# Kernel tuning notes

Measured on AMD Instinct MI355X. Metric: run time of the kernel, lower is better.

## Reference

```python
import jax, jax.numpy as jnp
import numpy as np

B, N, S, D1, D2 = 16, 4096, 1024, 128, 256
MLP = [256, 128]
BN_EPS = 1e-5


def setup_inputs() -> dict:
    key = jax.random.key(0)
    ks = jax.random.split(key, 12)
    inp = {
        "xyz1": jax.random.normal(ks[0], (B, 3, N), dtype=jnp.float32),
        "xyz2": jax.random.normal(ks[1], (B, 3, S), dtype=jnp.float32),
        "points1": jax.random.normal(ks[2], (B, D1, N), dtype=jnp.float32),
        "points2": jax.random.normal(ks[3], (B, D2, S), dtype=jnp.float32),
    }
    in_ch = D1 + D2  # 384
    chans = [in_ch] + MLP
    ki = 4
    for li in range(len(MLP)):
        cin, cout = chans[li], chans[li + 1]
        inp[f"w{li+1}"] = jax.random.normal(ks[ki], (cout, cin), dtype=jnp.float32) * (1.0 / np.sqrt(cin)); ki += 1
        inp[f"b{li+1}"] = jnp.zeros((cout,), dtype=jnp.float32)
        inp[f"g{li+1}"] = jnp.ones((cout,), dtype=jnp.float32)
        inp[f"beta{li+1}"] = jnp.zeros((cout,), dtype=jnp.float32)
    return inp


def _batchnorm1d(x, gamma, beta):
    # x: [B, C, N]; training-mode batch stats over (B, N)
    mean = jnp.mean(x, axis=(0, 2), keepdims=True)
    var = jnp.var(x, axis=(0, 2), keepdims=True)
    xhat = (x - mean) * jax.lax.rsqrt(var + BN_EPS)
    return xhat * gamma[None, :, None] + beta[None, :, None]


def reference(xyz1, xyz2, points1, points2, w1, b1, g1, beta1, w2, b2, g2, beta2):
    x1 = jnp.transpose(xyz1, (0, 2, 1))   # [B, N, 3]
    x2 = jnp.transpose(xyz2, (0, 2, 1))   # [B, S, 3]
    p2 = jnp.transpose(points2, (0, 2, 1))  # [B, S, D2]

    # squared pairwise distances [B, N, S]
    dists = jnp.sum((x1[:, :, None, :] - x2[:, None, :, :]) ** 2, axis=-1)
    # 3 smallest distances (original sorts then slices top-3)
    neg_d3, idx = jax.lax.top_k(-dists, 3)  # [B, N, 3]
    d3 = -neg_d3
    dist_recip = 1.0 / (d3 + 1e-8)
    weight = dist_recip / jnp.sum(dist_recip, axis=2, keepdims=True)  # [B, N, 3]

    # gather neighbor features: [B, N, 3, D2]
    feats = p2[jnp.arange(p2.shape[0])[:, None, None], idx]
    interp = jnp.sum(feats * weight[..., None], axis=2)  # [B, N, D2]

    p1 = jnp.transpose(points1, (0, 2, 1))  # [B, N, D1]
    new_points = jnp.concatenate([p1, interp], axis=-1)  # [B, N, D1+D2]
    x = jnp.transpose(new_points, (0, 2, 1))  # [B, C, N]

    for w, b, g, bt in ((w1, b1, g1, beta1), (w2, b2, g2, beta2)):
        x = jnp.einsum("oc,bcn->bon", w, x) + b[None, :, None]
        x = _batchnorm1d(x, g, bt)
        x = jax.nn.relu(x)
    return x
```

## Files before the change

### kernel.cpp

```cpp
#include <hip/hip_runtime.h>

typedef unsigned short u16;
typedef unsigned int   u32;
typedef __attribute__((ext_vector_type(8))) short bf16x8;
typedef __attribute__((ext_vector_type(8))) unsigned short u16x8;
typedef __attribute__((ext_vector_type(4))) float f32x4;

#define NB   16
#define NPTS 4096
#define SPTS 1024
#define BNT  65536

__device__ __forceinline__ float bf2f(u16 u){ return __uint_as_float(((u32)u)<<16); }
__device__ __forceinline__ u16 f2bf(float f){
  u32 u = __float_as_uint(f);
  return (u16)((u + 0x7FFFu + ((u>>16)&1u))>>16);
}

__global__ __launch_bounds__(256) void convw_k(const float* __restrict__ w1, const float* __restrict__ w2,
                                               u16* __restrict__ w1b, u16* __restrict__ w2b){
  int i = blockIdx.x*256 + threadIdx.x;
  if (i < 98304) w1b[i] = f2bf(w1[i]);
  else { int j = i - 98304; w2b[j] = f2bf(w2[j]); }
}

__global__ __launch_bounds__(256) void transpose_k(const float* __restrict__ in, u16* __restrict__ out,
                                                   int C, int S, int ostride){
  __shared__ float tl[64][65];
  int t = threadIdx.x;
  int b = blockIdx.y;
  int s0 = blockIdx.x * 64;
  for (int ct = 0; ct < C; ct += 64){
    __syncthreads();
    for (int i = t; i < 4096; i += 256){
      int sl = i & 63, cl = i >> 6;
      tl[sl][cl] = in[((size_t)b*C + ct + cl)*S + s0 + sl];
    }
    __syncthreads();
    for (int i = t; i < 4096; i += 256){
      int cl = i & 63, sl = i >> 6;
      out[((size_t)b*S + s0 + sl)*ostride + ct + cl] = f2bf(tl[sl][cl]);
    }
  }
}

__global__ __launch_bounds__(512) void knn_k(const float* __restrict__ xyz1, const float* __restrict__ xyz2,
                                             const u16* __restrict__ p2t, u16* __restrict__ X){
  __shared__ float4 sxyz[SPTS];
  __shared__ float  pd[8][3][64];
  __shared__ int    pi[8][3][64];
  __shared__ float  swts[3][64];
  __shared__ int    sidx[3][64];
  int t  = threadIdx.x;
  int b  = blockIdx.x >> 6;
  int n0 = (blockIdx.x & 63) << 6;
  const float* x2b = xyz2 + (size_t)b*3*SPTS;
  for (int s = t; s < SPTS; s += 512)
    sxyz[s] = make_float4(x2b[s], x2b[SPTS+s], x2b[2*SPTS+s], 0.f);
  int q = t & 63, g = t >> 6;
  const float* x1b = xyz1 + (size_t)b*3*NPTS;
  int n = n0 + q;
  float qx = x1b[n], qy = x1b[NPTS+n], qz = x1b[2*NPTS+n];
  __syncthreads();

  float d0=3.4e38f, d1=3.4e38f, d2=3.4e38f;
  int   i0=0, i1=0, i2=0;
  int sBeg = g << 7, sEnd = sBeg + 128;
  for (int s = sBeg; s < sEnd; ++s){
    float4 p = sxyz[s];
    float dist;
    {
      #pragma clang fp contract(off)
      float dx = qx - p.x, dy = qy - p.y, dz = qz - p.z;
      dist = ((dx*dx) + (dy*dy)) + (dz*dz);
    }
    if (dist < d2){
      bool c1 = dist < d1, c0 = dist < d0;
      d2 = c1 ? d1 : dist;                 i2 = c1 ? i1 : s;
      float nd1 = c1 ? (c0 ? d0 : dist) : d1;
      int   ni1 = c1 ? (c0 ? i0 : s)    : i1;
      d0 = c0 ? dist : d0;                 i0 = c0 ? s : i0;
      d1 = nd1;                            i1 = ni1;
    }
  }
  pd[g][0][q]=d0; pd[g][1][q]=d1; pd[g][2][q]=d2;
  pi[g][0][q]=i0; pi[g][1][q]=i1; pi[g][2][q]=i2;
  __syncthreads();

  if (t < 64){
    float m0=3.4e38f, m1=3.4e38f, m2=3.4e38f;
    int   j0=0, j1=0, j2=0;
    #pragma unroll
    for (int gg = 0; gg < 8; ++gg){
      #pragma unroll
      for (int p = 0; p < 3; ++p){
        float dist = pd[gg][p][t]; int s = pi[gg][p][t];
        if (dist < m2){
          bool c1 = dist < m1, c0 = dist < m0;
          m2 = c1 ? m1 : dist;                 j2 = c1 ? j1 : s;
          float nd1 = c1 ? (c0 ? m0 : dist) : m1;
          int   ni1 = c1 ? (c0 ? j0 : s)    : j1;
          m0 = c0 ? dist : m0;                 j0 = c0 ? s : j0;
          m1 = nd1;                            j1 = ni1;
        }
      }
    }
    float r0 = 1.f/(m0 + 1e-8f), r1 = 1.f/(m1 + 1e-8f), r2 = 1.f/(m2 + 1e-8f);
    float rs = (r0 + r1) + r2;
    swts[0][t] = r0/rs; swts[1][t] = r1/rs; swts[2][t] = r2/rs;
    sidx[0][t] = j0;    sidx[1][t] = j1;    sidx[2][t] = j2;
  }
  __syncthreads();

  int w = t >> 6, lane = t & 63;
  for (int qq = w*8; qq < w*8 + 8; ++qq){
    float wa = swts[0][qq], wb = swts[1][qq], wc = swts[2][qq];
    int   j0 = sidx[0][qq], j1 = sidx[1][qq], j2 = sidx[2][qq];
    const ushort4 u0 = *(const ushort4*)(p2t + (((size_t)b*SPTS + j0)<<8) + (lane<<2));
    const ushort4 u1 = *(const ushort4*)(p2t + (((size_t)b*SPTS + j1)<<8) + (lane<<2));
    const ushort4 u2 = *(const ushort4*)(p2t + (((size_t)b*SPTS + j2)<<8) + (lane<<2));
    ushort4 ov;
    ov.x = f2bf(wa*bf2f(u0.x) + wb*bf2f(u1.x) + wc*bf2f(u2.x));
    ov.y = f2bf(wa*bf2f(u0.y) + wb*bf2f(u1.y) + wc*bf2f(u2.y));
    ov.z = f2bf(wa*bf2f(u0.z) + wb*bf2f(u1.z) + wc*bf2f(u2.z));
    ov.w = f2bf(wa*bf2f(u0.w) + wb*bf2f(u1.w) + wc*bf2f(u2.w));
    *(ushort4*)(X + ((size_t)b*NPTS + n0 + qq)*384 + 128 + (lane<<2)) = ov;
  }
}


__global__ __launch_bounds__(256) void gemm1_k(const u16* __restrict__ A, const u16* __restrict__ Bw,
                                               u16* __restrict__ Cc,
                                               float* __restrict__ psum, float* __restrict__ psq){
  const int K = 384, Nn = 256;
  __shared__ u16 lA[64*64];
  __shared__ u16 lB[128*64];
  __shared__ float sums[128], sqs[128];
  int t = threadIdx.x, lane = t & 63, wid = t >> 6;
  int rowBase = blockIdx.x << 6, colBase = blockIdx.y << 7;
  int wm = wid >> 1, wn = wid & 1;

  const char* pA[2]; char* dA[2];
  #pragma unroll
  for (int j = 0; j < 2; ++j){
    int L = j*4096 + wid*1024 + lane*16;
    int row = L >> 7, kb = L & 127;
    int kbs = kb ^ ((row & 7) << 4);
    pA[j] = (const char*)A + ((size_t)(rowBase + row)*K)*2 + kbs;
    dA[j] = (char*)lA + j*4096 + wid*1024;
  }
  const char* pB[4]; char* dB[4];
  #pragma unroll
  for (int j = 0; j < 4; ++j){
    int L = j*4096 + wid*1024 + lane*16;
    int row = L >> 7, kb = L & 127;
    int kbs = kb ^ ((row & 7) << 4);
    pB[j] = (const char*)Bw + ((size_t)(colBase + row)*K)*2 + kbs;
    dB[j] = (char*)lB + j*4096 + wid*1024;
  }

  f32x4 z = {0.f,0.f,0.f,0.f};
  f32x4 acc[2][4];
  #pragma unroll
  for (int m = 0; m < 2; ++m)
    #pragma unroll
    for (int n = 0; n < 4; ++n) acc[m][n] = z;

  for (int kk = 0; kk < K; kk += 64){
    size_t ko = (size_t)kk * 2;
    #pragma unroll
    for (int j = 0; j < 2; ++j)
      __builtin_amdgcn_global_load_lds((const __attribute__((address_space(1))) void*)(pA[j] + ko),
                                       (__attribute__((address_space(3))) void*)dA[j], 16, 0, 0);
    #pragma unroll
    for (int j = 0; j < 4; ++j)
      __builtin_amdgcn_global_load_lds((const __attribute__((address_space(1))) void*)(pB[j] + ko),
                                       (__attribute__((address_space(3))) void*)dB[j], 16, 0, 0);
    __syncthreads();
    bf16x8 af[2][2], bfv[4][2];
    #pragma unroll
    for (int m = 0; m < 2; ++m){
      int row = wm*32 + m*16 + (lane & 15);
      int sw = (row & 7) << 4;
      #pragma unroll
      for (int ks = 0; ks < 2; ++ks){
        int kb = (ks*64 + ((lane >> 4) << 4)) ^ sw;
        af[m][ks] = *(const bf16x8*)((const char*)lA + row*128 + kb);
      }
    }
    #pragma unroll
    for (int n = 0; n < 4; ++n){
      int row = wn*64 + n*16 + (lane & 15);
      int sw = (row & 7) << 4;
      #pragma unroll
      for (int ks = 0; ks < 2; ++ks){
        int kb = (ks*64 + ((lane >> 4) << 4)) ^ sw;
        bfv[n][ks] = *(const bf16x8*)((const char*)lB + row*128 + kb);
      }
    }
    #pragma unroll
    for (int ks = 0; ks < 2; ++ks)
      #pragma unroll
      for (int m = 0; m < 2; ++m)
        #pragma unroll
        for (int n = 0; n < 4; ++n)
          acc[m][n] = __builtin_amdgcn_mfma_f32_16x16x32_bf16(af[m][ks], bfv[n][ks], acc[m][n], 0, 0, 0);
    __syncthreads();
  }

  if (t < 128){ sums[t] = 0.f; sqs[t] = 0.f; }
  __syncthreads();
  int colb = colBase + wn*64 + (lane & 15);
  int rowb = rowBase + wm*32 + ((lane >> 4) << 2);
  #pragma unroll
  for (int n = 0; n < 4; ++n){
    float s = 0.f, qq2 = 0.f;
    #pragma unroll
    for (int m = 0; m < 2; ++m){
      #pragma unroll
      for (int r = 0; r < 4; ++r){
        float v = acc[m][n][r];
        Cc[(size_t)(rowb + m*16 + r)*Nn + colb + n*16] = f2bf(v);
        s += v; qq2 += v*v;
      }
    }
    atomicAdd(&sums[wn*64 + n*16 + (lane & 15)], s);
    atomicAdd(&sqs [wn*64 + n*16 + (lane & 15)], qq2);
  }
  __syncthreads();
  if (t < 128){
    int c = colBase + t;
    psum[(size_t)c*1024 + blockIdx.x] = sums[t];
    psq [(size_t)c*1024 + blockIdx.x] = sqs[t];
  }
}

__global__ __launch_bounds__(256) void gemm2_k(const u16* __restrict__ A, const u16* __restrict__ Bw,
                                               u16* __restrict__ Cc,
                                               const float* __restrict__ sc, const float* __restrict__ sh,
                                               float* __restrict__ psum, float* __restrict__ psq){
  const int K = 256, Nn = 128;
  __shared__ u16 lA[64*64];
  __shared__ u16 lB[128*64];
  __shared__ float sums[128], sqs[128];
  int t = threadIdx.x, lane = t & 63, wid = t >> 6;
  int rowBase = blockIdx.x << 6;
  int wm = wid >> 1, wn = wid & 1;

  const char* pB[4]; char* dB[4];
  #pragma unroll
  for (int j = 0; j < 4; ++j){
    int L = j*4096 + wid*1024 + lane*16;
    int row = L >> 7, kb = L & 127;
    int kbs = kb ^ ((row & 7) << 4);
    pB[j] = (const char*)Bw + ((size_t)row*K)*2 + kbs;
    dB[j] = (char*)lB + j*4096 + wid*1024;
  }
  int arow = t & 63, achunk = t >> 6;
  const u16* pArow = A + (size_t)(rowBase + arow)*K + achunk*16;
  int asw = (arow & 7) << 4;
  char* wA0 = (char*)lA + arow*128 + (((achunk*32)      ) ^ asw);
  char* wA1 = (char*)lA + arow*128 + (((achunk*32) + 16 ) ^ asw);

  f32x4 z = {0.f,0.f,0.f,0.f};
  f32x4 acc[2][4];
  #pragma unroll
  for (int m = 0; m < 2; ++m)
    #pragma unroll
    for (int n = 0; n < 4; ++n) acc[m][n] = z;

  for (int kk = 0; kk < K; kk += 64){
    size_t ko = (size_t)kk * 2;
    #pragma unroll
    for (int j = 0; j < 4; ++j)
      __builtin_amdgcn_global_load_lds((const __attribute__((address_space(1))) void*)(pB[j] + ko),
                                       (__attribute__((address_space(3))) void*)dB[j], 16, 0, 0);
    u16x8 y0 = *(const u16x8*)(pArow + kk);
    u16x8 y1 = *(const u16x8*)(pArow + kk + 8);
    int k0 = kk + achunk*16;
    bf16x8 o0, o1;
    #pragma unroll
    for (int j = 0; j < 8; ++j){
      float v = bf2f((u16)y0[j]) * sc[k0 + j] + sh[k0 + j];
      o0[j] = (short)f2bf(fmaxf(v, 0.f));
    }
    #pragma unroll
    for (int j = 0; j < 8; ++j){
      float v = bf2f((u16)y1[j]) * sc[k0 + 8 + j] + sh[k0 + 8 + j];
      o1[j] = (short)f2bf(fmaxf(v, 0.f));
    }
    *(bf16x8*)wA0 = o0;
    *(bf16x8*)wA1 = o1;
    __syncthreads();
    bf16x8 af[2][2], bfv[4][2];
    #pragma unroll
    for (int m = 0; m < 2; ++m){
      int row = wm*32 + m*16 + (lane & 15);
      int sw = (row & 7) << 4;
      #pragma unroll
      for (int ks = 0; ks < 2; ++ks){
        int kb = (ks*64 + ((lane >> 4) << 4)) ^ sw;
        af[m][ks] = *(const bf16x8*)((const char*)lA + row*128 + kb);
      }
    }
    #pragma unroll
    for (int n = 0; n < 4; ++n){
      int row = wn*64 + n*16 + (lane & 15);
      int sw = (row & 7) << 4;
      #pragma unroll
      for (int ks = 0; ks < 2; ++ks){
        int kb = (ks*64 + ((lane >> 4) << 4)) ^ sw;
        bfv[n][ks] = *(const bf16x8*)((const char*)lB + row*128 + kb);
      }
    }
    #pragma unroll
    for (int ks = 0; ks < 2; ++ks)
      #pragma unroll
      for (int m = 0; m < 2; ++m)
        #pragma unroll
        for (int n = 0; n < 4; ++n)
          acc[m][n] = __builtin_amdgcn_mfma_f32_16x16x32_bf16(af[m][ks], bfv[n][ks], acc[m][n], 0, 0, 0);
    __syncthreads();
  }

  if (t < 128){ sums[t] = 0.f; sqs[t] = 0.f; }
  __syncthreads();
  int colb = wn*64 + (lane & 15);
  int rowb = rowBase + wm*32 + ((lane >> 4) << 2);
  #pragma unroll
  for (int n = 0; n < 4; ++n){
    float s = 0.f, qq2 = 0.f;
    #pragma unroll
    for (int m = 0; m < 2; ++m){
      #pragma unroll
      for (int r = 0; r < 4; ++r){
        float v = acc[m][n][r];
        Cc[(size_t)(rowb + m*16 + r)*Nn + colb + n*16] = f2bf(v);
        s += v; qq2 += v*v;
      }
    }
    atomicAdd(&sums[colb + n*16], s);
    atomicAdd(&sqs [colb + n*16], qq2);
  }
  __syncthreads();
  if (t < 128){
    psum[(size_t)t*1024 + blockIdx.x] = sums[t];
    psq [(size_t)t*1024 + blockIdx.x] = sqs[t];
  }
}

__global__ __launch_bounds__(256) void finalize2_k(const float* __restrict__ psum, const float* __restrict__ psq,
                                                   const float* __restrict__ g, const float* __restrict__ bet,
                                                   float* __restrict__ sc, float* __restrict__ sh){
  __shared__ float rs[256], rq[256];
  int c = blockIdx.x, t = threadIdx.x;
  float s = 0.f, q = 0.f;
  for (int rt = t; rt < 1024; rt += 256){
    s += psum[(size_t)c*1024 + rt];
    q += psq [(size_t)c*1024 + rt];
  }
  rs[t] = s; rq[t] = q;
  __syncthreads();
  for (int off = 128; off; off >>= 1){
    if (t < off){ rs[t] += rs[t+off]; rq[t] += rq[t+off]; }
    __syncthreads();
  }
  if (t == 0){
    const float inv = 1.f/65536.f;
    float mean = rs[0]*inv;
    float var  = rq[0]*inv - mean*mean;
    float rstd = rsqrtf(var + 1e-5f);
    float scl  = g[c]*rstd;
    sc[c] = scl;
    sh[c] = bet[c] - mean*scl;
  }
}

__global__ __launch_bounds__(256) void finalout_k(const u16* __restrict__ y2, const float* __restrict__ sc,
                                                  const float* __restrict__ sh, float* __restrict__ out){
  __shared__ float tl[128][65];
  int t  = threadIdx.x;
  int b  = blockIdx.x >> 6;
  int n0 = (blockIdx.x & 63) << 6;
  for (int i = t; i < 8192; i += 256){
    int r = i >> 7, c = i & 127;
    float v = bf2f(y2[((size_t)b*NPTS + n0 + r)*128 + c]);
    v = fmaxf(v*sc[c] + sh[c], 0.f);
    tl[c][r] = v;
  }
  __syncthreads();
  for (int i = t; i < 8192; i += 256){
    int o = i >> 6, j = i & 63;
    out[(size_t)b*128*NPTS + (size_t)o*NPTS + n0 + j] = tl[o][j];
  }
}

extern "C" void kernel_launch(void* const* d_in, const int* in_sizes, int n_in,
                              void* d_out, int out_size, void* d_ws, size_t ws_size,
                              hipStream_t stream) {
  const float* xyz1    = (const float*)d_in[0];
  const float* xyz2    = (const float*)d_in[1];
  const float* points1 = (const float*)d_in[2];
  const float* points2 = (const float*)d_in[3];
  const float* w1      = (const float*)d_in[4];
  const float* g1      = (const float*)d_in[6];
  const float* beta1   = (const float*)d_in[7];
  const float* w2      = (const float*)d_in[8];
  const float* g2      = (const float*)d_in[10];
  const float* beta2   = (const float*)d_in[11];

  char* ws = (char*)d_ws;
  u16*  X    = (u16*)ws;
  u16*  Y2   = (u16*)ws;
  u16*  Y1   = (u16*)(ws + 50331648);
  u16*  p2t  = (u16*)(ws + 83886080);
  u16*  w1b  = (u16*)(ws + 92274688);
  u16*  w2b  = (u16*)(ws + 92471296);
  float* psum1 = (float*)(ws + 83886080);
  float* psq1  = (float*)(ws + 84934656);
  float* psum2 = (float*)(ws + 85983232);
  float* psq2  = (float*)(ws + 86507520);
  float* sc1   = (float*)(ws + 87031808);
  float* sh1   = (float*)(ws + 87032832);
  float* sc2   = (float*)(ws + 87033856);
  float* sh2   = (float*)(ws + 87034368);

  convw_k<<<512, 256, 0, stream>>>(w1, w2, w1b, w2b);
  transpose_k<<<dim3(64, 16), 256, 0, stream>>>(points1, X,   128, NPTS, 384);
  transpose_k<<<dim3(16, 16), 256, 0, stream>>>(points2, p2t, 256, SPTS, 256);
  knn_k<<<1024, 512, 0, stream>>>(xyz1, xyz2, p2t, X);
  gemm1_k<<<dim3(1024, 2), 256, 0, stream>>>(X, w1b, Y1, psum1, psq1);
  finalize2_k<<<256, 256, 0, stream>>>(psum1, psq1, g1, beta1, sc1, sh1);
  gemm2_k<<<1024, 256, 0, stream>>>(Y1, w2b, Y2, sc1, sh1, psum2, psq2);
  finalize2_k<<<128, 256, 0, stream>>>(psum2, psq2, g2, beta2, sc2, sh2);
  finalout_k<<<1024, 256, 0, stream>>>(Y2, sc2, sh2, (float*)d_out);
}
```

Measured before the change: 154.9 us.

## Double-buffer GEMM K-loops, widen gemm1 tile, pack kNN distance+index into doubles

Both GEMM kernels now double-buffer their LDS tiles, so the next K-slice is prefetched with global_load_lds while MFMAs run on the current one. gemm1 covers all 256 output columns per block, which halves the grid and removes the repeated A-tile loads. The kNN top-3 packs the distance and index into one double and keeps a branchless fmin/fmax sorting network. Costs are more LDS and registers per block, which may lower occupancy, and the packed index overwrites low mantissa bits, so near-equal distances can tie-break differently.

```diff
diff --git a/kernel.cpp b/kernel.cpp
--- a/kernel.cpp
+++ b/kernel.cpp
@@ -2,6 +2,7 @@
 
 typedef unsigned short u16;
 typedef unsigned int   u32;
+typedef unsigned long long u64;
 typedef __attribute__((ext_vector_type(8))) short bf16x8;
 typedef __attribute__((ext_vector_type(8))) unsigned short u16x8;
 typedef __attribute__((ext_vector_type(4))) float f32x4;
@@ -10,6 +11,10 @@
 #define NPTS 4096
 #define SPTS 1024
 #define BNT  65536
+
+#define G2L(src, dst) __builtin_amdgcn_global_load_lds( \
+    (const __attribute__((address_space(1))) void*)(src), \
+    (__attribute__((address_space(3))) void*)(dst), 16, 0, 0)
 
 __device__ __forceinline__ float bf2f(u16 u){ return __uint_as_float(((u32)u)<<16); }
 __device__ __forceinline__ u16 f2bf(float f){
@@ -47,8 +52,7 @@
 __global__ __launch_bounds__(512) void knn_k(const float* __restrict__ xyz1, const float* __restrict__ xyz2,
                                              const u16* __restrict__ p2t, u16* __restrict__ X){
   __shared__ float4 sxyz[SPTS];
-  __shared__ float  pd[8][3][64];
-  __shared__ int    pi[8][3][64];
+  __shared__ double pp[8][3][64];
   __shared__ float  swts[3][64];
   __shared__ int    sidx[3][64];
   int t  = threadIdx.x;
@@ -63,10 +67,11 @@
   float qx = x1b[n], qy = x1b[NPTS+n], qz = x1b[2*NPTS+n];
   __syncthreads();
 
-  float d0=3.4e38f, d1=3.4e38f, d2=3.4e38f;
-  int   i0=0, i1=0, i2=0;
-  int sBeg = g << 7, sEnd = sBeg + 128;
-  for (int s = sBeg; s < sEnd; ++s){
+  double k0 = 1e300, k1 = 1e300, k2 = 1e300;
+  int sBeg = g << 7;
+  #pragma unroll 4
+  for (int sj = 0; sj < 128; ++sj){
+    int s = sBeg + sj;
     float4 p = sxyz[s];
     float dist;
     {
@@ -74,38 +79,33 @@
       float dx = qx - p.x, dy = qy - p.y, dz = qz - p.z;
       dist = ((dx*dx) + (dy*dy)) + (dz*dz);
     }
-    if (dist < d2){
-      bool c1 = dist < d1, c0 = dist < d0;
-      d2 = c1 ? d1 : dist;                 i2 = c1 ? i1 : s;
-      float nd1 = c1 ? (c0 ? d0 : dist) : d1;
-      int   ni1 = c1 ? (c0 ? i0 : s)    : i1;
-      d0 = c0 ? dist : d0;                 i0 = c0 ? s : i0;
-      d1 = nd1;                            i1 = ni1;
-    }
-  }
-  pd[g][0][q]=d0; pd[g][1][q]=d1; pd[g][2][q]=d2;
-  pi[g][0][q]=i0; pi[g][1][q]=i1; pi[g][2][q]=i2;
+    double pk = __longlong_as_double(__double_as_longlong((double)dist) | (long long)s);
+    double n2 = fmin(fmax(pk, k1), k2);
+    double n1 = fmin(fmax(pk, k0), k1);
+    double n0d = fmin(pk, k0);
+    k0 = n0d; k1 = n1; k2 = n2;
+  }
+  pp[g][0][q] = k0; pp[g][1][q] = k1; pp[g][2][q] = k2;
   __syncthreads();
 
   if (t < 64){
-    float m0=3.4e38f, m1=3.4e38f, m2=3.4e38f;
-    int   j0=0, j1=0, j2=0;
+    double m0 = 1e300, m1 = 1e300, m2 = 1e300;
     #pragma unroll
     for (int gg = 0; gg < 8; ++gg){
       #pragma unroll
       for (int p = 0; p < 3; ++p){
-        float dist = pd[gg][p][t]; int s = pi[gg][p][t];
-        if (dist < m2){
-          bool c1 = dist < m1, c0 = dist < m0;
-          m2 = c1 ? m1 : dist;                 j2 = c1 ? j1 : s;
-          float nd1 = c1 ? (c0 ? m0 : dist) : m1;
-          int   ni1 = c1 ? (c0 ? j0 : s)    : j1;
-          m0 = c0 ? dist : m0;                 j0 = c0 ? s : j0;
-          m1 = nd1;                            j1 = ni1;
-        }
-      }
-    }
-    float r0 = 1.f/(m0 + 1e-8f), r1 = 1.f/(m1 + 1e-8f), r2 = 1.f/(m2 + 1e-8f);
+        double pk = pp[gg][p][t];
+        double n2 = fmin(fmax(pk, m1), m2);
+        double n1 = fmin(fmax(pk, m0), m1);
+        double n0d = fmin(pk, m0);
+        m0 = n0d; m1 = n1; m2 = n2;
+      }
+    }
+    int j0 = (int)(__double_as_longlong(m0) & 1023);
+    int j1 = (int)(__double_as_longlong(m1) & 1023);
+    int j2 = (int)(__double_as_longlong(m2) & 1023);
+    float e0 = (float)m0, e1 = (float)m1, e2 = (float)m2;
+    float r0 = 1.f/(e0 + 1e-8f), r1 = 1.f/(e1 + 1e-8f), r2 = 1.f/(e2 + 1e-8f);
     float rs = (r0 + r1) + r2;
     swts[0][t] = r0/rs; swts[1][t] = r1/rs; swts[2][t] = r2/rs;
     sidx[0][t] = j0;    sidx[1][t] = j1;    sidx[2][t] = j2;
@@ -128,92 +128,89 @@
   }
 }
 
-
 __global__ __launch_bounds__(256) void gemm1_k(const u16* __restrict__ A, const u16* __restrict__ Bw,
                                                u16* __restrict__ Cc,
                                                float* __restrict__ psum, float* __restrict__ psq){
   const int K = 384, Nn = 256;
-  __shared__ u16 lA[64*64];
-  __shared__ u16 lB[128*64];
-  __shared__ float sums[128], sqs[128];
+  __shared__ u16 lA[2][64*64];
+  __shared__ u16 lB[2][256*64];
+  __shared__ float sums[256], sqs[256];
   int t = threadIdx.x, lane = t & 63, wid = t >> 6;
-  int rowBase = blockIdx.x << 6, colBase = blockIdx.y << 7;
+  int rowBase = blockIdx.x << 6;
   int wm = wid >> 1, wn = wid & 1;
 
-  const char* pA[2]; char* dA[2];
+  const char* pA[2]; int dAo[2];
   #pragma unroll
   for (int j = 0; j < 2; ++j){
-    int L = j*4096 + wid*1024 + lane*16;
+    int L = j*4096 + t*16;
     int row = L >> 7, kb = L & 127;
     int kbs = kb ^ ((row & 7) << 4);
     pA[j] = (const char*)A + ((size_t)(rowBase + row)*K)*2 + kbs;
-    dA[j] = (char*)lA + j*4096 + wid*1024;
-  }
-  const char* pB[4]; char* dB[4];
-  #pragma unroll
-  for (int j = 0; j < 4; ++j){
-    int L = j*4096 + wid*1024 + lane*16;
+    dAo[j] = j*4096 + wid*1024;
+  }
+  const char* pB[8]; int dBo[8];
+  #pragma unroll
+  for (int j = 0; j < 8; ++j){
+    int L = j*4096 + t*16;
     int row = L >> 7, kb = L & 127;
     int kbs = kb ^ ((row & 7) << 4);
-    pB[j] = (const char*)Bw + ((size_t)(colBase + row)*K)*2 + kbs;
-    dB[j] = (char*)lB + j*4096 + wid*1024;
+    pB[j] = (const char*)Bw + ((size_t)row*K)*2 + kbs;
+    dBo[j] = j*4096 + wid*1024;
   }
 
   f32x4 z = {0.f,0.f,0.f,0.f};
-  f32x4 acc[2][4];
+  f32x4 acc[2][8];
   #pragma unroll
   for (int m = 0; m < 2; ++m)
     #pragma unroll
-    for (int n = 0; n < 4; ++n) acc[m][n] = z;
-
-  for (int kk = 0; kk < K; kk += 64){
-    size_t ko = (size_t)kk * 2;
-    #pragma unroll
-    for (int j = 0; j < 2; ++j)
-      __builtin_amdgcn_global_load_lds((const __attribute__((address_space(1))) void*)(pA[j] + ko),
-                                       (__attribute__((address_space(3))) void*)dA[j], 16, 0, 0);
-    #pragma unroll
-    for (int j = 0; j < 4; ++j)
-      __builtin_amdgcn_global_load_lds((const __attribute__((address_space(1))) void*)(pB[j] + ko),
-                                       (__attribute__((address_space(3))) void*)dB[j], 16, 0, 0);
+    for (int n = 0; n < 8; ++n) acc[m][n] = z;
+
+  #pragma unroll
+  for (int j = 0; j < 2; ++j) G2L(pA[j], (char*)lA[0] + dAo[j]);
+  #pragma unroll
+  for (int j = 0; j < 8; ++j) G2L(pB[j], (char*)lB[0] + dBo[j]);
+  __syncthreads();
+
+  #pragma unroll
+  for (int kt = 0; kt < 6; ++kt){
+    const int cur = kt & 1;
+    if (kt < 5){
+      size_t ko = (size_t)(kt + 1) * 128;
+      #pragma unroll
+      for (int j = 0; j < 2; ++j) G2L(pA[j] + ko, (char*)lA[cur^1] + dAo[j]);
+      #pragma unroll
+      for (int j = 0; j < 8; ++j) G2L(pB[j] + ko, (char*)lB[cur^1] + dBo[j]);
+    }
+    #pragma unroll
+    for (int ks = 0; ks < 2; ++ks){
+      bf16x8 af[2];
+      #pragma unroll
+      for (int m = 0; m < 2; ++m){
+        int row = wm*32 + m*16 + (lane & 15);
+        int sw = (row & 7) << 4;
+        int kb = (ks*64 + ((lane >> 4) << 4)) ^ sw;
+        af[m] = *(const bf16x8*)((const char*)lA[cur] + row*128 + kb);
+      }
+      #pragma unroll
+      for (int n = 0; n < 8; ++n){
+        int row = wn*128 + n*16 + (lane & 15);
+        int sw = (row & 7) << 4;
+        int kb = (ks*64 + ((lane >> 4) << 4)) ^ sw;
+        bf16x8 bv = *(const bf16x8*)((const char*)lB[cur] + row*128 + kb);
+        #pragma unroll
+        for (int m = 0; m < 2; ++m)
+          acc[m][n] = __builtin_amdgcn_mfma_f32_16x16x32_bf16(af[m], bv, acc[m][n], 0, 0, 0);
+      }
+    }
     __syncthreads();
-    bf16x8 af[2][2], bfv[4][2];
-    #pragma unroll
-    for (int m = 0; m < 2; ++m){
-      int row = wm*32 + m*16 + (lane & 15);
-      int sw = (row & 7) << 4;
-      #pragma unroll
-      for (int ks = 0; ks < 2; ++ks){
-        int kb = (ks*64 + ((lane >> 4) << 4)) ^ sw;
-        af[m][ks] = *(const bf16x8*)((const char*)lA + row*128 + kb);
-      }
-    }
-    #pragma unroll
-    for (int n = 0; n < 4; ++n){
-      int row = wn*64 + n*16 + (lane & 15);
-      int sw = (row & 7) << 4;
-      #pragma unroll
-      for (int ks = 0; ks < 2; ++ks){
-        int kb = (ks*64 + ((lane >> 4) << 4)) ^ sw;
-        bfv[n][ks] = *(const bf16x8*)((const char*)lB + row*128 + kb);
-      }
-    }
-    #pragma unroll
-    for (int ks = 0; ks < 2; ++ks)
-      #pragma unroll
-      for (int m = 0; m < 2; ++m)
-        #pragma unroll
-        for (int n = 0; n < 4; ++n)
-          acc[m][n] = __builtin_amdgcn_mfma_f32_16x16x32_bf16(af[m][ks], bfv[n][ks], acc[m][n], 0, 0, 0);
-    __syncthreads();
-  }
-
-  if (t < 128){ sums[t] = 0.f; sqs[t] = 0.f; }
-  __syncthreads();
-  int colb = colBase + wn*64 + (lane & 15);
+  }
+
+  sums[t] = 0.f; sqs[t] = 0.f;
+  __syncthreads();
+  int colb = wn*128 + (lane & 15);
   int rowb = rowBase + wm*32 + ((lane >> 4) << 2);
   #pragma unroll
-  for (int n = 0; n < 4; ++n){
+  for (int n = 0; n < 8; ++n){
     float s = 0.f, qq2 = 0.f;
     #pragma unroll
     for (int m = 0; m < 2; ++m){
@@ -224,15 +221,12 @@
         s += v; qq2 += v*v;
       }
     }
-    atomicAdd(&sums[wn*64 + n*16 + (lane & 15)], s);
-    atomicAdd(&sqs [wn*64 + n*16 + (lane & 15)], qq2);
-  }
-  __syncthreads();
-  if (t < 128){
-    int c = colBase + t;
-    psum[(size_t)c*1024 + blockIdx.x] = sums[t];
-    psq [(size_t)c*1024 + blockIdx.x] = sqs[t];
-  }
+    atomicAdd(&sums[colb + n*16], s);
+    atomicAdd(&sqs [colb + n*16], qq2);
+  }
+  __syncthreads();
+  psum[(size_t)t*1024 + blockIdx.x] = sums[t];
+  psq [(size_t)t*1024 + blockIdx.x] = sqs[t];
 }
 
 __global__ __launch_bounds__(256) void gemm2_k(const u16* __restrict__ A, const u16* __restrict__ Bw,
@@ -240,27 +234,27 @@
                                                const float* __restrict__ sc, const float* __restrict__ sh,
                                                float* __restrict__ psum, float* __restrict__ psq){
   const int K = 256, Nn = 128;
-  __shared__ u16 lA[64*64];
-  __shared__ u16 lB[128*64];
+  __shared__ u16 lA[2][64*64];
+  __shared__ u16 lB[2][128*64];
   __shared__ float sums[128], sqs[128];
   int t = threadIdx.x, lane = t & 63, wid = t >> 6;
   int rowBase = blockIdx.x << 6;
   int wm = wid >> 1, wn = wid & 1;
 
-  const char* pB[4]; char* dB[4];
+  const char* pB[4]; int dBo[4];
   #pragma unroll
   for (int j = 0; j < 4; ++j){
-    int L = j*4096 + wid*1024 + lane*16;
+    int L = j*4096 + t*16;
     int row = L >> 7, kb = L & 127;
     int kbs = kb ^ ((row & 7) << 4);
     pB[j] = (const char*)Bw + ((size_t)row*K)*2 + kbs;
-    dB[j] = (char*)lB + j*4096 + wid*1024;
+    dBo[j] = j*4096 + wid*1024;
   }
   int arow = t & 63, achunk = t >> 6;
   const u16* pArow = A + (size_t)(rowBase + arow)*K + achunk*16;
   int asw = (arow & 7) << 4;
-  char* wA0 = (char*)lA + arow*128 + (((achunk*32)      ) ^ asw);
-  char* wA1 = (char*)lA + arow*128 + (((achunk*32) + 16 ) ^ asw);
+  int wAo0 = arow*128 + ((achunk*32)      ^ asw);
+  int wAo1 = arow*128 + ((achunk*32 + 16) ^ asw);
 
   f32x4 z = {0.f,0.f,0.f,0.f};
   f32x4 acc[2][4];
@@ -269,15 +263,12 @@
     #pragma unroll
     for (int n = 0; n < 4; ++n) acc[m][n] = z;
 
-  for (int kk = 0; kk < K; kk += 64){
-    size_t ko = (size_t)kk * 2;
-    #pragma unroll
-    for (int j = 0; j < 4; ++j)
-      __builtin_amdgcn_global_load_lds((const __attribute__((address_space(1))) void*)(pB[j] + ko),
-                                       (__attribute__((address_space(3))) void*)dB[j], 16, 0, 0);
-    u16x8 y0 = *(const u16x8*)(pArow + kk);
-    u16x8 y1 = *(const u16x8*)(pArow + kk + 8);
-    int k0 = kk + achunk*16;
+  #pragma unroll
+  for (int j = 0; j < 4; ++j) G2L(pB[j], (char*)lB[0] + dBo[j]);
+  {
+    u16x8 y0 = *(const u16x8*)(pArow);
+    u16x8 y1 = *(const u16x8*)(pArow + 8);
+    int k0 = achunk*16;
     bf16x8 o0, o1;
     #pragma unroll
     for (int j = 0; j < 8; ++j){
@@ -289,37 +280,59 @@
       float v = bf2f((u16)y1[j]) * sc[k0 + 8 + j] + sh[k0 + 8 + j];
       o1[j] = (short)f2bf(fmaxf(v, 0.f));
     }
-    *(bf16x8*)wA0 = o0;
-    *(bf16x8*)wA1 = o1;
-    __syncthreads();
-    bf16x8 af[2][2], bfv[4][2];
-    #pragma unroll
-    for (int m = 0; m < 2; ++m){
-      int row = wm*32 + m*16 + (lane & 15);
-      int sw = (row & 7) << 4;
-      #pragma unroll
-      for (int ks = 0; ks < 2; ++ks){
+    *(bf16x8*)((char*)lA[0] + wAo0) = o0;
+    *(bf16x8*)((char*)lA[0] + wAo1) = o1;
+  }
+  __syncthreads();
+
+  #pragma unroll
+  for (int kt = 0; kt < 4; ++kt){
+    const int cur = kt & 1;
+    u16x8 ny0 = {}, ny1 = {};
+    if (kt < 3){
+      size_t ko = (size_t)(kt + 1) * 128;
+      #pragma unroll
+      for (int j = 0; j < 4; ++j) G2L(pB[j] + ko, (char*)lB[cur^1] + dBo[j]);
+      ny0 = *(const u16x8*)(pArow + (kt+1)*64);
+      ny1 = *(const u16x8*)(pArow + (kt+1)*64 + 8);
+    }
+    #pragma unroll
+    for (int ks = 0; ks < 2; ++ks){
+      bf16x8 af[2];
+      #pragma unroll
+      for (int m = 0; m < 2; ++m){
+        int row = wm*32 + m*16 + (lane & 15);
+        int sw = (row & 7) << 4;
         int kb = (ks*64 + ((lane >> 4) << 4)) ^ sw;
-        af[m][ks] = *(const bf16x8*)((const char*)lA + row*128 + kb);
-      }
-    }
-    #pragma unroll
-    for (int n = 0; n < 4; ++n){
-      int row = wn*64 + n*16 + (lane & 15);
-      int sw = (row & 7) << 4;
-      #pragma unroll
-      for (int ks = 0; ks < 2; ++ks){
+        af[m] = *(const bf16x8*)((const char*)lA[cur] + row*128 + kb);
+      }
+      #pragma unroll
+      for (int n = 0; n < 4; ++n){
+        int row = wn*64 + n*16 + (lane & 15);
+        int sw = (row & 7) << 4;
         int kb = (ks*64 + ((lane >> 4) << 4)) ^ sw;
-        bfv[n][ks] = *(const bf16x8*)((const char*)lB + row*128 + kb);
-      }
-    }
-    #pragma unroll
-    for (int ks = 0; ks < 2; ++ks)
-      #pragma unroll
-      for (int m = 0; m < 2; ++m)
+        bf16x8 bv = *(const bf16x8*)((const char*)lB[cur] + row*128 + kb);
         #pragma unroll
-        for (int n = 0; n < 4; ++n)
-          acc[m][n] = __builtin_amdgcn_mfma_f32_16x16x32_bf16(af[m][ks], bfv[n][ks], acc[m][n], 0, 0, 0);
+        for (int m = 0; m < 2; ++m)
+          acc[m][n] = __builtin_amdgcn_mfma_f32_16x16x32_bf16(af[m], bv, acc[m][n], 0, 0, 0);
+      }
+    }
+    if (kt < 3){
+      int k0 = (kt+1)*64 + achunk*16;
+      bf16x8 o0, o1;
+      #pragma unroll
+      for (int j = 0; j < 8; ++j){
+        float v = bf2f((u16)ny0[j]) * sc[k0 + j] + sh[k0 + j];
+        o0[j] = (short)f2bf(fmaxf(v, 0.f));
+      }
+      #pragma unroll
+      for (int j = 0; j < 8; ++j){
+        float v = bf2f((u16)ny1[j]) * sc[k0 + 8 + j] + sh[k0 + 8 + j];
+        o1[j] = (short)f2bf(fmaxf(v, 0.f));
+      }
+      *(bf16x8*)((char*)lA[cur^1] + wAo0) = o0;
+      *(bf16x8*)((char*)lA[cur^1] + wAo1) = o1;
+    }
     __syncthreads();
   }
 
@@ -429,7 +442,7 @@
   transpose_k<<<dim3(64, 16), 256, 0, stream>>>(points1, X,   128, NPTS, 384);
   transpose_k<<<dim3(16, 16), 256, 0, stream>>>(points2, p2t, 256, SPTS, 256);
   knn_k<<<1024, 512, 0, stream>>>(xyz1, xyz2, p2t, X);
-  gemm1_k<<<dim3(1024, 2), 256, 0, stream>>>(X, w1b, Y1, psum1, psq1);
+  gemm1_k<<<1024, 256, 0, stream>>>(X, w1b, Y1, psum1, psq1);
   finalize2_k<<<256, 256, 0, stream>>>(psum1, psq1, g1, beta1, sc1, sh1);
   gemm2_k<<<1024, 256, 0, stream>>>(Y1, w2b, Y2, sc1, sh1, psum2, psq2);
   finalize2_k<<<128, 256, 0, stream>>>(psum2, psq2, g2, beta2, sc2, sh2);
```

Result: slower. 174.1 us (+12.4%).
